# Performance work log

Measured on AMD Instinct MI355X. Metric: run time of the kernel, lower is better.

Reference implementation:

```python
import jax, jax.numpy as jnp
import numpy as np

C_M, C_H, C_Z = 256, 32, 128
LN_EPS = 1e-5
MASK_EPS = 1e-8


def setup_inputs() -> dict:
    key = jax.random.key(0)
    ks = jax.random.split(key, 8)
    B, N, L = 1, 128, 256
    m = jax.random.normal(ks[0], (B, N, L, C_M), dtype=jnp.float32)
    msa_mask = jnp.ones((B, N, L), dtype=jnp.float32)
    # parameters
    ln_gamma = jnp.ones((C_M,), dtype=jnp.float32)
    ln_beta = jnp.zeros((C_M,), dtype=jnp.float32)
    sa = 1.0 / np.sqrt(C_M)
    Wa = jax.random.uniform(ks[1], (C_M, C_H), jnp.float32, -sa, sa)
    ba = jax.random.uniform(ks[2], (C_H,), jnp.float32, -sa, sa)
    Wb = jax.random.uniform(ks[3], (C_M, C_H), jnp.float32, -sa, sa)
    bb = jax.random.uniform(ks[4], (C_H,), jnp.float32, -sa, sa)
    so = 1.0 / np.sqrt(C_H * C_H)
    Wo = jax.random.uniform(ks[5], (C_H * C_H, C_Z), jnp.float32, -so, so)
    bo = jax.random.uniform(ks[6], (C_Z,), jnp.float32, -so, so)
    return {"m": m, "msa_mask": msa_mask, "ln_gamma": ln_gamma, "ln_beta": ln_beta,
            "Wa": Wa, "ba": ba, "Wb": Wb, "bb": bb, "Wo": Wo, "bo": bo}


def reference(m, msa_mask, ln_gamma, ln_beta, Wa, ba, Wb, bb, Wo, bo):
    B, N, L, _ = m.shape
    # LayerNorm over c_m
    mu = jnp.mean(m, axis=-1, keepdims=True)
    var = jnp.mean(jnp.square(m - mu), axis=-1, keepdims=True)
    x = (m - mu) * jax.lax.rsqrt(var + LN_EPS) * ln_gamma + ln_beta
    a = x @ Wa + ba                       # [B,N,L,c_h]
    b = x @ Wb + bb                       # [B,N,L,c_h]
    mk = msa_mask[..., None]
    a = a * mk
    b = b * mk
    # outer product mean over MSA depth: [B,L,L,c_h,c_h]
    outer = jnp.einsum('bnic,bnjd->bijcd', a, b)
    pair_mask = jnp.einsum('bni,bnj->bij', msa_mask, msa_mask)
    outer = outer / (pair_mask[..., None, None] + MASK_EPS)
    outer = outer.reshape(B, L, L, -1)    # [B,L,L,c_h*c_h]
    z_update = outer @ Wo + bo            # [B,L,L,c_z]
    return z_update
```

## Files before the change

kernel.cpp:

```cpp
#include <hip/hip_runtime.h>
#include <hip/hip_bf16.h>


typedef __attribute__((ext_vector_type(8))) short bf8_t;
typedef __attribute__((ext_vector_type(4))) float f32x4;

__device__ __forceinline__ unsigned short f2bf(float f) {
    unsigned int u = __float_as_uint(f);
    u += 0x7fffu + ((u >> 16) & 1u);
    return (unsigned short)(u >> 16);
}
__device__ __forceinline__ unsigned int pack2(float a, float b) {
    return (unsigned int)f2bf(a) | ((unsigned int)f2bf(b) << 16);
}

__global__ __launch_bounds__(256) void k_prep(const float* __restrict__ Wa,
                                              const float* __restrict__ Wb,
                                              unsigned short* __restrict__ WTb) {
    int u = blockIdx.x * 256 + threadIdx.x;
    int h = u >> 8, c = u & 255;
    float v = (h < 32) ? Wa[c * 32 + h] : Wb[c * 32 + (h - 32)];
    WTb[u] = f2bf(v);
}

__global__ __launch_bounds__(256) void k_ln_proj(
    const float* __restrict__ gm, const float* __restrict__ gmask,
    const float* __restrict__ gamma, const float* __restrict__ beta,
    const unsigned short* __restrict__ WTb,
    const float* __restrict__ ba, const float* __restrict__ bb,
    const float* __restrict__ Wo,
    unsigned short* __restrict__ aT, unsigned short* __restrict__ bT,
    unsigned short* __restrict__ W2, float* __restrict__ pmr)
{
    const int tid = threadIdx.x;
    const int tail = (int)blockIdx.x - 2048;
    if (tail >= 0) {
        if (tail < 512) {
            int u = tail * 256 + tid;
            int k = u >> 7, z = u & 127;
            int c = k >> 5, d = k & 31;
            int kp = d * 32 + c;
            int dst = (((z >> 4) * 32 + (kp >> 5)) * 16 + (z & 15)) * 32
                      + ((kp >> 3) & 3) * 8 + (kp & 7);
            W2[dst] = f2bf(Wo[u]);
        } else {
            int u = (tail - 512) * 256 + tid;
            int i = u >> 8, j = u & 255;
            float s = 0.f;
            #pragma unroll 8
            for (int n = 0; n < 128; n++)
                s += gmask[n * 256 + i] * gmask[n * 256 + j];
            pmr[u] = 1.f / (s + 1e-8f);
        }
        return;
    }

    __shared__ __align__(16) unsigned short xlb[16 * 256];
    __shared__ float vl[16 * 64];
    const int lane = tid & 63, w = tid >> 6;
    const int l = blockIdx.x & 255, n0 = ((int)blockIdx.x >> 8) << 4;

    const float4 g4  = ((const float4*)gamma)[lane];
    const float4 be4 = ((const float4*)beta)[lane];

    #pragma unroll
    for (int j = 0; j < 4; j++) {
        int row = w * 4 + j;
        int n = n0 + row;
        float4 v = ((const float4*)(gm + ((size_t)n * 256 + l) * 256))[lane];
        float s = v.x + v.y + v.z + v.w;
        float q = v.x * v.x + v.y * v.y + v.z * v.z + v.w * v.w;
        #pragma unroll
        for (int off = 1; off < 64; off <<= 1) {
            s += __shfl_xor(s, off);
            q += __shfl_xor(q, off);
        }
        float mean = s * (1.f / 256.f);
        float var = fmaxf(q * (1.f / 256.f) - mean * mean, 0.f);
        float rstd = rsqrtf(var + 1e-5f);
        float x0 = (v.x - mean) * rstd * g4.x + be4.x;
        float x1 = (v.y - mean) * rstd * g4.y + be4.y;
        float x2 = (v.z - mean) * rstd * g4.z + be4.z;
        float x3 = (v.w - mean) * rstd * g4.w + be4.w;
        int c8s = lane ^ ((row & 7) << 1);
        *(uint2*)((char*)xlb + row * 512 + (c8s << 3)) =
            make_uint2(pack2(x0, x1), pack2(x2, x3));
    }
    __syncthreads();

    const int kg = lane >> 4, r16 = lane & 15;
    const int h = w * 16 + r16;
    f32x4 acc = {0.f, 0.f, 0.f, 0.f};
    #pragma unroll
    for (int ks = 0; ks < 8; ks++) {
        int c8 = ks * 8 + kg * 2;
        bf8_t af = *(const bf8_t*)((char*)xlb + r16 * 512 +
                                   ((c8 ^ ((r16 & 7) << 1)) << 3));
        bf8_t wf = *(const bf8_t*)(WTb + (size_t)h * 256 + ks * 32 + kg * 8);
        acc = __builtin_amdgcn_mfma_f32_16x16x32_bf16(af, wf, acc, 0, 0, 0);
    }
    float bias = (h < 32) ? ba[h] : bb[h - 32];
    #pragma unroll
    for (int r = 0; r < 4; r++) {
        int nrow = kg * 4 + r;
        float mk = gmask[(size_t)(n0 + nrow) * 256 + l];
        vl[nrow * 64 + h] = (acc[r] + bias) * mk;
    }
    __syncthreads();

    if (tid < 128) {
        int row = tid >> 1, half = tid & 1;
        int hh = row & 31;
        unsigned short* dst = (row < 32) ? aT : bT;
        unsigned int pk[4];
        #pragma unroll
        for (int jj = 0; jj < 4; jj++)
            pk[jj] = pack2(vl[(half * 8 + 2 * jj) * 64 + row],
                           vl[(half * 8 + 2 * jj + 1) * 64 + row]);
        *(uint4*)(dst + ((size_t)l * 32 + hh) * 128 + n0 + half * 8) =
            make_uint4(pk[0], pk[1], pk[2], pk[3]);
    }
}

__global__ __launch_bounds__(512) void k_outer(
    const unsigned short* __restrict__ aT, const unsigned short* __restrict__ bT,
    const unsigned short* __restrict__ W2, const float* __restrict__ pmr,
    const float* __restrict__ bo, float* __restrict__ out)
{
    __shared__ __align__(16) char smem[32768];
    const int tid = threadIdx.x, lane = tid & 63, w = tid >> 6;
    const int wr = w >> 2, wc = w & 3;
    const int tj = blockIdx.x & 63, ti = blockIdx.x >> 6;
    const int kg = lane >> 4, r16 = lane & 15;

    f32x4 acc[4][2];
    #pragma unroll
    for (int mt = 0; mt < 4; mt++)
        #pragma unroll
        for (int nt = 0; nt < 2; nt++)
            acc[mt][nt] = (f32x4){0.f, 0.f, 0.f, 0.f};

    const uint4* gA = (const uint4*)(aT + (size_t)ti * 16384);
    const uint4* gB = (const uint4*)(bT + (size_t)tj * 16384);

    #pragma unroll
    for (int half = 0; half < 2; half++) {
        #pragma unroll
        for (int k = 0; k < 2; k++) {
            int g = k * 512 + tid;
            int row = g >> 3, ch = g & 7;
            int dsto = row * 128 + ((ch ^ (row & 7)) << 4);
            *(uint4*)(smem + dsto)         = gA[row * 16 + half * 8 + ch];
            *(uint4*)(smem + 16384 + dsto) = gB[row * 16 + half * 8 + ch];
        }
        __syncthreads();
        #pragma unroll
        for (int ks2 = 0; ks2 < 2; ks2++) {
            bf8_t af[4], bfr[2];
            int ch = ks2 * 4 + kg;
            #pragma unroll
            for (int mt = 0; mt < 4; mt++) {
                int mm = wr * 64 + mt * 16 + r16;
                af[mt] = *(const bf8_t*)(smem + mm * 128 + ((ch ^ (mm & 7)) << 4));
            }
            #pragma unroll
            for (int nt = 0; nt < 2; nt++) {
                int nn = wc * 32 + nt * 16 + r16;
                bfr[nt] = *(const bf8_t*)(smem + 16384 + nn * 128 + ((ch ^ (nn & 7)) << 4));
            }
            #pragma unroll
            for (int mt = 0; mt < 4; mt++)
                #pragma unroll
                for (int nt = 0; nt < 2; nt++)
                    acc[mt][nt] = __builtin_amdgcn_mfma_f32_16x16x32_bf16(
                        af[mt], bfr[nt], acc[mt][nt], 0, 0, 0);
        }
        __syncthreads();
    }

    unsigned short* O2b = (unsigned short*)smem;
    #pragma unroll
    for (int mt = 0; mt < 4; mt++) {
        int mmb = wr * 64 + mt * 16 + kg * 4;
        #pragma unroll
        for (int nt = 0; nt < 2; nt++) {
            int nn = wc * 32 + nt * 16 + r16;
            int p  = ((mmb >> 5) << 2) | (nn >> 5);
            int k2 = ((nn & 31) << 5) | (mmb & 31);
            int c2 = k2 >> 3;
            int pc = c2 ^ ((c2 >> 3) & 7) ^ (p & 7);
            *(uint2*)(O2b + p * 1024 + pc * 8 + (k2 & 7)) =
                make_uint2(pack2(acc[mt][nt][0], acc[mt][nt][1]),
                           pack2(acc[mt][nt][2], acc[mt][nt][3]));
        }
    }
    __syncthreads();

    f32x4 acc2 = {0.f, 0.f, 0.f, 0.f};
    const unsigned short* O2r = O2b + r16 * 1024;
    const int psw = r16 & 7;
    const unsigned short* wz = W2 + (size_t)w * 16384 + r16 * 32 + kg * 8;
    #pragma unroll 8
    for (int s = 0; s < 32; s++) {
        int c2 = s * 4 + kg;
        int pc = c2 ^ ((c2 >> 3) & 7) ^ psw;
        bf8_t av = *(const bf8_t*)(O2r + pc * 8);
        bf8_t wf = *(const bf8_t*)(wz + s * 512);
        acc2 = __builtin_amdgcn_mfma_f32_16x16x32_bf16(av, wf, acc2, 0, 0, 0);
    }

    const int i0 = ti * 4, j0 = tj * 4;
    const int z = w * 16 + r16;
    const float boz = bo[z];
    #pragma unroll
    for (int r = 0; r < 4; r++) {
        int p = kg * 4 + r;
        int i = i0 + (p >> 2), j = j0 + (p & 3);
        float recip = pmr[i * 256 + j];
        out[((size_t)(i * 256 + j)) * 128 + z] = acc2[r] * recip + boz;
    }
}

extern "C" void kernel_launch(void* const* d_in, const int* in_sizes, int n_in,
                              void* d_out, int out_size, void* d_ws, size_t ws_size,
                              hipStream_t stream)
{
    const float* m    = (const float*)d_in[0];
    const float* mask = (const float*)d_in[1];
    const float* gam  = (const float*)d_in[2];
    const float* bet  = (const float*)d_in[3];
    const float* Wa   = (const float*)d_in[4];
    const float* ba   = (const float*)d_in[5];
    const float* Wb   = (const float*)d_in[6];
    const float* bb   = (const float*)d_in[7];
    const float* Wo   = (const float*)d_in[8];
    const float* bo   = (const float*)d_in[9];
    float* out = (float*)d_out;

    unsigned short* aT  = (unsigned short*)d_ws;
    unsigned short* bT  = aT + 8192 * 128;
    unsigned short* W2  = bT + 8192 * 128;
    unsigned short* WTb = W2 + 128 * 1024;
    float* pmr = (float*)(WTb + 64 * 256);

    k_prep   <<<  64, 256, 0, stream>>>(Wa, Wb, WTb);
    k_ln_proj<<<2816, 256, 0, stream>>>(m, mask, gam, bet, WTb, ba, bb, Wo,
                                        aT, bT, W2, pmr);
    k_outer  <<<4096, 512, 0, stream>>>(aT, bT, W2, pmr, bo, out);
}
```

Measured before the change: 184.9 us.

## Double i-tile per block in k_outer, use async global-to-LDS loads

```diff
diff --git a/kernel.cpp b/kernel.cpp
--- a/kernel.cpp
+++ b/kernel.cpp
@@ -12,6 +12,12 @@
 }
 __device__ __forceinline__ unsigned int pack2(float a, float b) {
     return (unsigned int)f2bf(a) | ((unsigned int)f2bf(b) << 16);
+}
+
+__device__ __forceinline__ void cp16_async(const void* g, void* l) {
+    __builtin_amdgcn_global_load_lds(
+        (const __attribute__((address_space(1))) unsigned int*)g,
+        (__attribute__((address_space(3))) unsigned int*)l, 16, 0, 0);
 }
 
 __global__ __launch_bounds__(256) void k_prep(const float* __restrict__ Wa,
@@ -122,58 +128,64 @@
     }
 }
 
-__global__ __launch_bounds__(512) void k_outer(
+__global__ __launch_bounds__(512, 4) void k_outer(
     const unsigned short* __restrict__ aT, const unsigned short* __restrict__ bT,
     const unsigned short* __restrict__ W2, const float* __restrict__ pmr,
     const float* __restrict__ bo, float* __restrict__ out)
 {
-    __shared__ __align__(16) char smem[32768];
+    __shared__ __align__(16) char smem[65536];
     const int tid = threadIdx.x, lane = tid & 63, w = tid >> 6;
-    const int wr = w >> 2, wc = w & 3;
+    const int wr = w >> 1, wc = w & 1;
     const int tj = blockIdx.x & 63, ti = blockIdx.x >> 6;
     const int kg = lane >> 4, r16 = lane & 15;
 
-    f32x4 acc[4][2];
+    f32x4 acc[4][4];
     #pragma unroll
     for (int mt = 0; mt < 4; mt++)
         #pragma unroll
-        for (int nt = 0; nt < 2; nt++)
+        for (int nt = 0; nt < 4; nt++)
             acc[mt][nt] = (f32x4){0.f, 0.f, 0.f, 0.f};
 
-    const uint4* gA = (const uint4*)(aT + (size_t)ti * 16384);
+    const uint4* gA = (const uint4*)(aT + (size_t)ti * 32768);
     const uint4* gB = (const uint4*)(bT + (size_t)tj * 16384);
 
     #pragma unroll
     for (int half = 0; half < 2; half++) {
         #pragma unroll
-        for (int k = 0; k < 2; k++) {
-            int g = k * 512 + tid;
-            int row = g >> 3, ch = g & 7;
-            int dsto = row * 128 + ((ch ^ (row & 7)) << 4);
-            *(uint4*)(smem + dsto)         = gA[row * 16 + half * 8 + ch];
-            *(uint4*)(smem + 16384 + dsto) = gB[row * 16 + half * 8 + ch];
+        for (int t = 0; t < 4; t++) {
+            int q = w * 256 + t * 64 + lane;
+            int row = q >> 3, c = q & 7;
+            cp16_async(gA + row * 16 + half * 8 + (c ^ (row & 7)),
+                       smem + ((w * 256 + t * 64) << 4));
+        }
+        #pragma unroll
+        for (int t = 0; t < 2; t++) {
+            int q = w * 128 + t * 64 + lane;
+            int row = q >> 3, c = q & 7;
+            cp16_async(gB + row * 16 + half * 8 + (c ^ (row & 7)),
+                       smem + 32768 + ((w * 128 + t * 64) << 4));
         }
         __syncthreads();
+
         #pragma unroll
         for (int ks2 = 0; ks2 < 2; ks2++) {
-            bf8_t af[4], bfr[2];
             int ch = ks2 * 4 + kg;
+            bf8_t af[4];
             #pragma unroll
             for (int mt = 0; mt < 4; mt++) {
                 int mm = wr * 64 + mt * 16 + r16;
                 af[mt] = *(const bf8_t*)(smem + mm * 128 + ((ch ^ (mm & 7)) << 4));
             }
             #pragma unroll
-            for (int nt = 0; nt < 2; nt++) {
-                int nn = wc * 32 + nt * 16 + r16;
-                bfr[nt] = *(const bf8_t*)(smem + 16384 + nn * 128 + ((ch ^ (nn & 7)) << 4));
+            for (int nt = 0; nt < 4; nt++) {
+                int nn = wc * 64 + nt * 16 + r16;
+                bf8_t bfr = *(const bf8_t*)(smem + 32768 + nn * 128 +
+                                            ((ch ^ (nn & 7)) << 4));
+                #pragma unroll
+                for (int mt = 0; mt < 4; mt++)
+                    acc[mt][nt] = __builtin_amdgcn_mfma_f32_16x16x32_bf16(
+                        af[mt], bfr, acc[mt][nt], 0, 0, 0);
             }
-            #pragma unroll
-            for (int mt = 0; mt < 4; mt++)
-                #pragma unroll
-                for (int nt = 0; nt < 2; nt++)
-                    acc[mt][nt] = __builtin_amdgcn_mfma_f32_16x16x32_bf16(
-                        af[mt], bfr[nt], acc[mt][nt], 0, 0, 0);
         }
         __syncthreads();
     }
@@ -183,8 +195,8 @@
     for (int mt = 0; mt < 4; mt++) {
         int mmb = wr * 64 + mt * 16 + kg * 4;
         #pragma unroll
-        for (int nt = 0; nt < 2; nt++) {
-            int nn = wc * 32 + nt * 16 + r16;
+        for (int nt = 0; nt < 4; nt++) {
+            int nn = wc * 64 + nt * 16 + r16;
             int p  = ((mmb >> 5) << 2) | (nn >> 5);
             int k2 = ((nn & 31) << 5) | (mmb & 31);
             int c2 = k2 >> 3;
@@ -196,29 +208,45 @@
     }
     __syncthreads();
 
-    f32x4 acc2 = {0.f, 0.f, 0.f, 0.f};
+    f32x4 acc2[2];
+    acc2[0] = (f32x4){0.f, 0.f, 0.f, 0.f};
+    acc2[1] = (f32x4){0.f, 0.f, 0.f, 0.f};
     const unsigned short* O2r = O2b + r16 * 1024;
     const int psw = r16 & 7;
     const unsigned short* wz = W2 + (size_t)w * 16384 + r16 * 32 + kg * 8;
-    #pragma unroll 8
-    for (int s = 0; s < 32; s++) {
+    bf8_t wf = *(const bf8_t*)(wz);
+    #pragma unroll 4
+    for (int s = 0; s < 31; s++) {
+        bf8_t wfn = *(const bf8_t*)(wz + (s + 1) * 512);
         int c2 = s * 4 + kg;
         int pc = c2 ^ ((c2 >> 3) & 7) ^ psw;
-        bf8_t av = *(const bf8_t*)(O2r + pc * 8);
-        bf8_t wf = *(const bf8_t*)(wz + s * 512);
-        acc2 = __builtin_amdgcn_mfma_f32_16x16x32_bf16(av, wf, acc2, 0, 0, 0);
-    }
-
-    const int i0 = ti * 4, j0 = tj * 4;
+        bf8_t a0 = *(const bf8_t*)(O2r + pc * 8);
+        bf8_t a1 = *(const bf8_t*)(O2r + 16384 + pc * 8);
+        acc2[0] = __builtin_amdgcn_mfma_f32_16x16x32_bf16(a0, wf, acc2[0], 0, 0, 0);
+        acc2[1] = __builtin_amdgcn_mfma_f32_16x16x32_bf16(a1, wf, acc2[1], 0, 0, 0);
+        wf = wfn;
+    }
+    {
+        int c2 = 31 * 4 + kg;
+        int pc = c2 ^ ((c2 >> 3) & 7) ^ psw;
+        bf8_t a0 = *(const bf8_t*)(O2r + pc * 8);
+        bf8_t a1 = *(const bf8_t*)(O2r + 16384 + pc * 8);
+        acc2[0] = __builtin_amdgcn_mfma_f32_16x16x32_bf16(a0, wf, acc2[0], 0, 0, 0);
+        acc2[1] = __builtin_amdgcn_mfma_f32_16x16x32_bf16(a1, wf, acc2[1], 0, 0, 0);
+    }
+
+    const int i0 = ti * 8, j0 = tj * 4;
     const int z = w * 16 + r16;
     const float boz = bo[z];
     #pragma unroll
-    for (int r = 0; r < 4; r++) {
-        int p = kg * 4 + r;
-        int i = i0 + (p >> 2), j = j0 + (p & 3);
-        float recip = pmr[i * 256 + j];
-        out[((size_t)(i * 256 + j)) * 128 + z] = acc2[r] * recip + boz;
-    }
+    for (int mt = 0; mt < 2; mt++)
+        #pragma unroll
+        for (int r = 0; r < 4; r++) {
+            int p = mt * 16 + kg * 4 + r;
+            int i = i0 + (p >> 2), j = j0 + (p & 3);
+            float recip = pmr[i * 256 + j];
+            out[((size_t)(i * 256 + j)) * 128 + z] = acc2[mt][r] * recip + boz;
+        }
 }
 
 extern "C" void kernel_launch(void* const* d_in, const int* in_sizes, int n_in,
@@ -246,5 +274,5 @@
     k_prep   <<<  64, 256, 0, stream>>>(Wa, Wb, WTb);
     k_ln_proj<<<2816, 256, 0, stream>>>(m, mask, gam, bet, WTb, ba, bb, Wo,
                                         aT, bT, W2, pmr);
-    k_outer  <<<4096, 512, 0, stream>>>(aT, bT, W2, pmr, bo, out);
-}
+    k_outer  <<<2048, 512, 0, stream>>>(aT, bT, W2, pmr, bo, out);
+}
```

Result: faster. 161.2 us (-12.8%).
